# Kernel tuning notes

Measured on AMD Instinct MI355X. Metric: run time of the kernel, lower is better.

The kernel has to match this reference:

```python
import jax, jax.numpy as jnp
import numpy as np

NUM_LAYERS = 2
D = 128
H = 4
L = 16  # context window length
EPS = 1e-6


def _ln(x, g, b):
    mu = jnp.mean(x, -1, keepdims=True)
    v = jnp.mean((x - mu) ** 2, -1, keepdims=True)
    return (x - mu) / jnp.sqrt(v + EPS) * g + b


def _lin(x, W, b):
    # torch Linear / 1x1 Conv2d convention: W is [out, in]
    return jnp.einsum('...i,oi->...o', x, W) + b


def _context_attention(x, Lw):
    # x: [b, m, t, d]; front zero-pad time by Lw-1, sliding-window attention.
    # Note: padded zero keys get logit 0 and DO participate in the softmax
    # (faithful to the original, which does not mask the padding).
    b, m, t, d = x.shape
    xp = jnp.pad(x, ((0, 0), (0, 0), (Lw - 1, 0), (0, 0)))
    idx = jnp.arange(t)[:, None] + jnp.arange(Lw)[None, :]  # [t, Lw]
    win = xp[:, :, idx, :]                                   # [b,m,t,Lw,d]
    s = jnp.einsum('bmtd,bmtld->bmtl', x, win) / jnp.sqrt(jnp.asarray(d, x.dtype))
    w = jax.nn.softmax(s, -1)
    return jnp.einsum('bmtl,bmtld->bmtd', w, win)


def _mha(y, Wq, bq, Wk, bk, Wv, bv, Wfc, bfc):
    b, m, t, d = y.shape
    dk = d // H
    q = _lin(y, Wq, bq)   # 1x1 conv == pointwise linear
    k = _lin(y, Wk, bk)
    v = _lin(y, Wv, bv)
    cq = _context_attention(q, L).reshape(b, m, t, H, dk).transpose(0, 1, 3, 2, 4)
    ck = _context_attention(k, L).reshape(b, m, t, H, dk).transpose(0, 1, 3, 2, 4)
    vh = v.reshape(b, m, t, H, dk).transpose(0, 1, 3, 2, 4)  # [b,m,h,t,dk]
    scale = jnp.sqrt(jnp.asarray(dk, y.dtype))
    s = jnp.einsum('bmhqd,bmhkd->bmhqk', cq, ck) / scale
    a = jax.nn.softmax(s, -1)
    x = jnp.einsum('bmhqk,bmhkd->bmhqd', a, vh)   # [b,m,h,t,dk]
    x = x.transpose(0, 1, 3, 2, 4)                # [b,m,t,h,dk]
    # relation attention across assets m
    xr = x.transpose(0, 2, 3, 1, 4)               # [b,t,h,m,dk]
    sr = jnp.einsum('bthqd,bthkd->bthqk', xr, xr) / scale
    ar = jax.nn.softmax(sr, -1)
    xr = jnp.einsum('bthqk,bthkd->bthqd', ar, xr) # [b,t,h,m,dk]
    x = xr.transpose(0, 3, 1, 2, 4)               # [b,m,t,h,dk]
    return _lin(x.reshape(b, m, t, d), Wfc, bfc)


def setup_inputs() -> dict:
    key = jax.random.key(0)
    ks = jax.random.split(key, 16)
    sc = D ** -0.5
    NL = NUM_LAYERS
    inp = {
        'x':   jax.random.normal(ks[0], (2, 32, 512, D), jnp.float32),
        'Wq':  jax.random.normal(ks[1], (NL, D, D)) * sc,
        'bq':  jnp.zeros((NL, D)),
        'Wk':  jax.random.normal(ks[2], (NL, D, D)) * sc,
        'bk':  jnp.zeros((NL, D)),
        'Wv':  jax.random.normal(ks[3], (NL, D, D)) * sc,
        'bv':  jnp.zeros((NL, D)),
        'Wfc': jax.random.normal(ks[4], (NL, D, D)) * sc,
        'bfc': jnp.zeros((NL, D)),
        'W1':  jax.random.normal(ks[5], (NL, 4 * D, D)) * sc,
        'b1':  jnp.zeros((NL, 4 * D)),
        'W2':  jax.random.normal(ks[6], (NL, D, 4 * D)) * (4 * D) ** -0.5,
        'b2':  jnp.zeros((NL, D)),
        'g1':  jnp.ones((NL, D)),  'be1': jnp.zeros((NL, D)),
        'g2':  jnp.ones((NL, D)),  'be2': jnp.zeros((NL, D)),
        'gf':  jnp.ones((D,)),     'bef': jnp.zeros((D,)),
    }
    return inp


def reference(x, Wq, bq, Wk, bk, Wv, bv, Wfc, bfc, W1, b1, W2, b2,
              g1, be1, g2, be2, gf, bef):
    for i in range(NUM_LAYERS):
        # sublayer 0: pre-LN self-attention + residual (dropout=0)
        y = _mha(_ln(x, g1[i], be1[i]), Wq[i], bq[i], Wk[i], bk[i],
                 Wv[i], bv[i], Wfc[i], bfc[i])
        x = x + y
        # sublayer 1: pre-LN FFN + residual
        z = _ln(x, g2[i], be2[i])
        x = x + _lin(jax.nn.relu(_lin(z, W1[i], b1[i])), W2[i], b2[i])
    return _ln(x, gf, bef)
```

## Files before the change

### kernel.cpp

```cpp
#include <hip/hip_runtime.h>
#include <hip/hip_bf16.h>
#include <math.h>

#define B 2
#define M 32
#define T 512
#define D 128
#define H 4
#define DK 32
#define NTOK (B*M*T)

using s16x8 = __attribute__((ext_vector_type(8))) short;
using s16x4 = __attribute__((ext_vector_type(4))) short;
using f32x4 = __attribute__((ext_vector_type(4))) float;

__device__ __forceinline__ short f2bf(float x) {
    union { float f; unsigned u; } a; a.f = x;
    unsigned r = a.u + 0x7fffu + ((a.u >> 16) & 1u);
    return (short)(r >> 16);
}
__device__ __forceinline__ unsigned pkbf(float lo, float hi) {
    union { __hip_bfloat162 h; unsigned u; } c;
    c.h = __float22bfloat162_rn(float2{lo, hi});
    return c.u;
}

__global__ __launch_bounds__(256) void cvt_all_kernel(const float* __restrict__ Wq, const float* __restrict__ Wk,
                                                      const float* __restrict__ Wv, const float* __restrict__ Wfc,
                                                      const float* __restrict__ W1, const float* __restrict__ W2,
                                                      short* __restrict__ dst)
{
    int i = (blockIdx.x * 256 + threadIdx.x) * 4;
    if (i >= 393216) return;
    const float* src; int off;
    if (i < 131072) {
        int wsel = i >> 15; off = i & 32767;
        src = (wsel == 0) ? Wq : (wsel == 1) ? Wk : (wsel == 2) ? Wv : Wfc;
    } else if (i < 262144) { src = W1; off = i - 131072; }
    else                   { src = W2; off = i - 262144; }
    float4 v = *(const float4*)(src + off);
    ushort4 u;
    u.x = (unsigned short)f2bf(v.x); u.y = (unsigned short)f2bf(v.y);
    u.z = (unsigned short)f2bf(v.z); u.w = (unsigned short)f2bf(v.w);
    *(ushort4*)(dst + i) = u;
}

__global__ __launch_bounds__(256) void ln_kernel(const float* __restrict__ in, float* __restrict__ outf,
                                                 const float* __restrict__ g, const float* __restrict__ b)
{
    int wave = threadIdx.x >> 6;
    int lane = threadIdx.x & 63;
    int row  = blockIdx.x * 4 + wave;
    const float* rp = in + (size_t)row * D;
    float v0 = rp[lane], v1 = rp[lane + 64];
    float s = v0 + v1, ss = v0 * v0 + v1 * v1;
    #pragma unroll
    for (int off = 32; off; off >>= 1) { s += __shfl_xor(s, off); ss += __shfl_xor(ss, off); }
    float mu  = s * (1.0f / 128.0f);
    float var = ss * (1.0f / 128.0f) - mu * mu;
    float rs  = rsqrtf(var + 1e-6f);
    float* op = outf + (size_t)row * D;
    op[lane]      = (v0 - mu) * rs * g[lane]      + b[lane];
    op[lane + 64] = (v1 - mu) * rs * g[lane + 64] + b[lane + 64];
}

#define KP 136

#define LN_STAGE(XPTR, GPTR, BEPTR)                                              \
    {                                                                            \
        const float* xp = (XPTR) + (size_t)(rowBase + sr) * D + sq * 32;         \
        float4 xv[8];                                                            \
        _Pragma("unroll")                                                        \
        for (int j = 0; j < 8; j++) xv[j] = *(const float4*)(xp + j * 4);        \
        float s = 0.0f, ss = 0.0f;                                               \
        _Pragma("unroll")                                                        \
        for (int j = 0; j < 8; j++) {                                            \
            s  += xv[j].x + xv[j].y + xv[j].z + xv[j].w;                         \
            ss += xv[j].x*xv[j].x + xv[j].y*xv[j].y + xv[j].z*xv[j].z + xv[j].w*xv[j].w; \
        }                                                                        \
        s  += __shfl_xor(s, 1);  s  += __shfl_xor(s, 2);                         \
        ss += __shfl_xor(ss, 1); ss += __shfl_xor(ss, 2);                        \
        float mu  = s * (1.0f / 128.0f);                                         \
        float var = ss * (1.0f / 128.0f) - mu * mu;                              \
        float rs  = rsqrtf(var + 1e-6f);                                         \
        const float* gp  = (GPTR) + sq * 32;                                     \
        const float* bep = (BEPTR) + sq * 32;                                    \
        short* asd = &As[sr * KP + sq * 32];                                     \
        _Pragma("unroll")                                                        \
        for (int c = 0; c < 4; c++) {                                            \
            float4 a0 = xv[2*c], a1 = xv[2*c+1];                                 \
            float4 g0 = *(const float4*)(gp + c * 8);                            \
            float4 g1 = *(const float4*)(gp + c * 8 + 4);                        \
            float4 b0 = *(const float4*)(bep + c * 8);                           \
            float4 b1 = *(const float4*)(bep + c * 8 + 4);                       \
            union { unsigned u[4]; s16x8 v8; } pu;                               \
            pu.u[0] = pkbf((a0.x-mu)*rs*g0.x+b0.x, (a0.y-mu)*rs*g0.y+b0.y);      \
            pu.u[1] = pkbf((a0.z-mu)*rs*g0.z+b0.z, (a0.w-mu)*rs*g0.w+b0.w);      \
            pu.u[2] = pkbf((a1.x-mu)*rs*g1.x+b1.x, (a1.y-mu)*rs*g1.y+b1.y);      \
            pu.u[3] = pkbf((a1.z-mu)*rs*g1.z+b1.z, (a1.w-mu)*rs*g1.w+b1.w);      \
            *(s16x8*)(asd + c * 8) = pu.v8;                                      \
        }                                                                        \
    }

__global__ __launch_bounds__(512) void qkv_ln_kernel(const float* __restrict__ X,
                                                     const float* __restrict__ g, const float* __restrict__ be,
                                                     const short* __restrict__ Wq, const short* __restrict__ Wk,
                                                     const short* __restrict__ Wv,
                                                     const float* __restrict__ bq, const float* __restrict__ bk,
                                                     const float* __restrict__ bv,
                                                     short* __restrict__ Qo, short* __restrict__ Ko,
                                                     short* __restrict__ Vo)
{
    __shared__ short As[128 * KP];
    __shared__ short Ws[3][128 * KP];
    const int tid = threadIdx.x;
    const int rowBase = blockIdx.x * 128;
    const int sr = tid >> 2, sq = tid & 3;
    const int w = tid >> 6, l = tid & 63;
    const int lg = l >> 4, lr = l & 15;
    const int wr = w >> 2, wc = w & 3;

    const short* wsrc[3] = { Wq, Wk, Wv };
    const float* bsrc[3] = { bq, bk, bv };
    short*       osrc[3] = { Qo, Ko, Vo };

    #pragma unroll
    for (int gsel = 0; gsel < 3; gsel++) {
        const short* wp = wsrc[gsel] + (size_t)sr * D + sq * 32;
        short* wsd = &Ws[gsel][sr * KP + sq * 32];
        #pragma unroll
        for (int i = 0; i < 4; i++) *(s16x8*)(wsd + i * 8) = *(const s16x8*)(wp + i * 8);
    }
    LN_STAGE(X, g, be)
    __syncthreads();

    for (int gsel = 0; gsel < 3; gsel++) {
        f32x4 acc[4][2];
        #pragma unroll
        for (int qi = 0; qi < 4; qi++)
            #pragma unroll
            for (int nj = 0; nj < 2; nj++)
                acc[qi][nj] = (f32x4){0.0f, 0.0f, 0.0f, 0.0f};
        #pragma unroll
        for (int kk = 0; kk < 4; kk++) {
            s16x8 af[4], bfr[2];
            #pragma unroll
            for (int qi = 0; qi < 4; qi++)
                af[qi] = *(const s16x8*)&As[(wr * 64 + qi * 16 + lr) * KP + kk * 32 + lg * 8];
            #pragma unroll
            for (int nj = 0; nj < 2; nj++)
                bfr[nj] = *(const s16x8*)&Ws[gsel][(wc * 32 + nj * 16 + lr) * KP + kk * 32 + lg * 8];
            #pragma unroll
            for (int qi = 0; qi < 4; qi++)
                #pragma unroll
                for (int nj = 0; nj < 2; nj++)
                    acc[qi][nj] = __builtin_amdgcn_mfma_f32_16x16x32_bf16(af[qi], bfr[nj], acc[qi][nj], 0, 0, 0);
        }
        #pragma unroll
        for (int nj = 0; nj < 2; nj++) {
            int col = wc * 32 + nj * 16 + lr;
            float bb = bsrc[gsel][col];
            #pragma unroll
            for (int qi = 0; qi < 4; qi++) {
                #pragma unroll
                for (int rr = 0; rr < 4; rr++) {
                    int row = rowBase + wr * 64 + qi * 16 + lg * 4 + rr;
                    osrc[gsel][(size_t)row * D + col] = f2bf(acc[qi][nj][rr] + bb);
                }
            }
        }
    }
}

__global__ __launch_bounds__(512) void mlp1_ln_kernel(const float* __restrict__ X,
                                                      const float* __restrict__ g, const float* __restrict__ be,
                                                      const short* __restrict__ W1, const float* __restrict__ b1,
                                                      short* __restrict__ Hb)
{
    __shared__ short As[128 * KP];
    __shared__ short Ws[128 * KP];
    const int tid = threadIdx.x;
    const int rowBase = blockIdx.x * 128;
    const int sr = tid >> 2, sq = tid & 3;
    const int w = tid >> 6, l = tid & 63;
    const int lg = l >> 4, lr = l & 15;
    const int wr = w >> 2, wc = w & 3;

    LN_STAGE(X, g, be)

    for (int ct = 0; ct < 4; ct++) {
        s16x8 wv4[4];
        const short* wp = W1 + (size_t)(ct * 128 + sr) * D + sq * 32;
        #pragma unroll
        for (int i = 0; i < 4; i++) wv4[i] = *(const s16x8*)(wp + i * 8);
        __syncthreads();
        short* wsd = &Ws[sr * KP + sq * 32];
        #pragma unroll
        for (int i = 0; i < 4; i++) *(s16x8*)(wsd + i * 8) = wv4[i];
        __syncthreads();

        f32x4 acc[4][2];
        #pragma unroll
        for (int qi = 0; qi < 4; qi++)
            #pragma unroll
            for (int nj = 0; nj < 2; nj++)
                acc[qi][nj] = (f32x4){0.0f, 0.0f, 0.0f, 0.0f};
        #pragma unroll
        for (int kk = 0; kk < 4; kk++) {
            s16x8 af[4], bfr[2];
            #pragma unroll
            for (int qi = 0; qi < 4; qi++)
                af[qi] = *(const s16x8*)&As[(wr * 64 + qi * 16 + lr) * KP + kk * 32 + lg * 8];
            #pragma unroll
            for (int nj = 0; nj < 2; nj++)
                bfr[nj] = *(const s16x8*)&Ws[(wc * 32 + nj * 16 + lr) * KP + kk * 32 + lg * 8];
            #pragma unroll
            for (int qi = 0; qi < 4; qi++)
                #pragma unroll
                for (int nj = 0; nj < 2; nj++)
                    acc[qi][nj] = __builtin_amdgcn_mfma_f32_16x16x32_bf16(af[qi], bfr[nj], acc[qi][nj], 0, 0, 0);
        }
        #pragma unroll
        for (int nj = 0; nj < 2; nj++) {
            int col = ct * 128 + wc * 32 + nj * 16 + lr;
            float bb = b1[col];
            #pragma unroll
            for (int qi = 0; qi < 4; qi++) {
                #pragma unroll
                for (int rr = 0; rr < 4; rr++) {
                    int row = rowBase + wr * 64 + qi * 16 + lg * 4 + rr;
                    Hb[(size_t)row * 512 + col] = f2bf(fmaxf(acc[qi][nj][rr] + bb, 0.0f));
                }
            }
        }
    }
}

template<int DIN>
__global__ __launch_bounds__(512) void gemm_bf16_kernel(const short* __restrict__ A, const short* __restrict__ W,
                                                        const float* __restrict__ bias, const float* __restrict__ res,
                                                        float* __restrict__ outf, int Dout)
{
    __shared__ short As[128 * KP];
    __shared__ short Ws[128 * KP];
    const int tid = threadIdx.x;
    const int rowBase = blockIdx.y * 128;
    const int colBase = blockIdx.x * 128;
    const int sr = tid >> 2, sq = tid & 3;
    const int w = tid >> 6, l = tid & 63;
    const int lg = l >> 4, lr = l & 15;
    const int wr = w >> 2, wc = w & 3;

    f32x4 acc[4][2];
    #pragma unroll
    for (int qi = 0; qi < 4; qi++)
        #pragma unroll
        for (int nj = 0; nj < 2; nj++)
            acc[qi][nj] = (f32x4){0.0f, 0.0f, 0.0f, 0.0f};

    const short* ap = A + (size_t)(rowBase + sr) * DIN + sq * 32;
    const short* wp = W + (size_t)(colBase + sr) * DIN + sq * 32;
    short* asd = &As[sr * KP + sq * 32];
    short* wsd = &Ws[sr * KP + sq * 32];

    #pragma unroll
    for (int kt = 0; kt < DIN / 128; kt++) {
        s16x8 av[4], wv[4];
        #pragma unroll
        for (int i = 0; i < 4; i++) {
            av[i] = *(const s16x8*)(ap + kt * 128 + i * 8);
            wv[i] = *(const s16x8*)(wp + kt * 128 + i * 8);
        }
        if (kt) __syncthreads();
        #pragma unroll
        for (int i = 0; i < 4; i++) {
            *(s16x8*)(asd + i * 8) = av[i];
            *(s16x8*)(wsd + i * 8) = wv[i];
        }
        __syncthreads();
        #pragma unroll
        for (int kk = 0; kk < 4; kk++) {
            s16x8 af[4], bfr[2];
            #pragma unroll
            for (int qi = 0; qi < 4; qi++)
                af[qi] = *(const s16x8*)&As[(wr * 64 + qi * 16 + lr) * KP + kk * 32 + lg * 8];
            #pragma unroll
            for (int nj = 0; nj < 2; nj++)
                bfr[nj] = *(const s16x8*)&Ws[(wc * 32 + nj * 16 + lr) * KP + kk * 32 + lg * 8];
            #pragma unroll
            for (int qi = 0; qi < 4; qi++)
                #pragma unroll
                for (int nj = 0; nj < 2; nj++)
                    acc[qi][nj] = __builtin_amdgcn_mfma_f32_16x16x32_bf16(af[qi], bfr[nj], acc[qi][nj], 0, 0, 0);
        }
    }

    #pragma unroll
    for (int nj = 0; nj < 2; nj++) {
        int col = colBase + wc * 32 + nj * 16 + lr;
        float bb = bias[col];
        #pragma unroll
        for (int qi = 0; qi < 4; qi++) {
            #pragma unroll
            for (int rr = 0; rr < 4; rr++) {
                int row = rowBase + wr * 64 + qi * 16 + lg * 4 + rr;
                size_t o = (size_t)row * Dout + col;
                outf[o] = acc[qi][nj][rr] + bb + res[o];
            }
        }
    }
}

#define XSP 136
#define XTP 84
__global__ __launch_bounds__(256) void ctx_mfma_kernel(const short* __restrict__ in0, short* __restrict__ out0,
                                                       const short* __restrict__ in1, short* __restrict__ out1)
{
    __shared__ short Xs[80 * XSP];
    __shared__ short Xt[128 * XTP];

    const short* in  = blockIdx.y ? in1 : in0;
    short*       out = blockIdx.y ? out1 : out0;
    int bm = blockIdx.x >> 3;
    int t0 = (blockIdx.x & 7) * 64;
    int tid = threadIdx.x;
    const short* base = in + (size_t)bm * T * D;

    #pragma unroll
    for (int it = 0; it < 5; it++) {
        int idx = it * 256 + tid;
        int row = idx >> 4, c16 = idx & 15;
        int t = t0 - 16 + row;
        s16x8 v = {0, 0, 0, 0, 0, 0, 0, 0};
        if (t >= 0) v = *(const s16x8*)(base + (size_t)t * D + c16 * 8);
        *(s16x8*)&Xs[row * XSP + c16 * 8] = v;
    }
    __syncthreads();
    #pragma unroll
    for (int it = 0; it < 5; it++) {
        int task = it * 256 + tid;
        int g = task / 80, row = task % 80;
        s16x8 v = *(const s16x8*)&Xs[row * XSP + g * 8];
        #pragma unroll
        for (int j = 0; j < 8; j++) Xt[(g * 8 + j) * XTP + row] = v[j];
    }
    __syncthreads();

    int w = tid >> 6, l = tid & 63;
    int lg = l >> 4, lr = l & 15;
    f32x4 zacc = {0.0f, 0.0f, 0.0f, 0.0f};
    const float C1 = 0.0883883476483184f * 1.4426950408889634f;

    s16x8 qf[4];
    #pragma unroll
    for (int kd = 0; kd < 4; kd++)
        qf[kd] = *(const s16x8*)&Xs[(16 + w * 16 + lr) * XSP + kd * 32 + lg * 8];

    f32x4 sacc[2];
    #pragma unroll
    for (int s = 0; s < 2; s++) {
        f32x4 a = zacc;
        #pragma unroll
        for (int kd = 0; kd < 4; kd++) {
            s16x8 kf = *(const s16x8*)&Xs[(w * 16 + s * 16 + lr) * XSP + kd * 32 + lg * 8];
            a = __builtin_amdgcn_mfma_f32_16x16x32_bf16(kf, qf[kd], a, 0, 0, 0);
        }
        sacc[s] = a;
    }

    float p[2][4];
    float mx = -1e30f;
    #pragma unroll
    for (int s = 0; s < 2; s++)
        #pragma unroll
        for (int r = 0; r < 4; r++) {
            int dlt = s * 16 + lg * 4 + r - 16 - lr;
            float val = (dlt >= -15 && dlt <= 0) ? sacc[s][r] : -1e30f;
            p[s][r] = val;
            mx = fmaxf(mx, val);
        }
    mx = fmaxf(mx, __shfl_xor(mx, 16));
    mx = fmaxf(mx, __shfl_xor(mx, 32));
    float mc = mx * C1;
    float ps = 0.0f;
    #pragma unroll
    for (int s = 0; s < 2; s++)
        #pragma unroll
        for (int r = 0; r < 4; r++) {
            float e = exp2f(fmaf(p[s][r], C1, -mc));
            p[s][r] = e;
            ps += e;
        }
    ps += __shfl_xor(ps, 16);
    ps += __shfl_xor(ps, 32);

    union { unsigned u[4]; s16x8 v8; } pu;
    pu.u[0] = pkbf(p[0][0], p[0][1]);
    pu.u[1] = pkbf(p[0][2], p[0][3]);
    pu.u[2] = pkbf(p[1][0], p[1][1]);
    pu.u[3] = pkbf(p[1][2], p[1][3]);
    s16x8 pf = pu.v8;

    float rl = 1.0f / ps;
    short* op = out + (size_t)(bm * T + t0 + w * 16 + lr) * D;
    #pragma unroll
    for (int dt = 0; dt < 8; dt++) {
        const short* vb = &Xt[(dt * 16 + lr) * XTP + w * 16 + lg * 4];
        s16x4 a = *(const s16x4*)(vb);
        s16x4 b = *(const s16x4*)(vb + 16);
        s16x8 vf = __builtin_shufflevector(a, b, 0, 1, 2, 3, 4, 5, 6, 7);
        f32x4 Oa = __builtin_amdgcn_mfma_f32_16x16x32_bf16(vf, pf, zacc, 0, 0, 0);
        union { unsigned u[2]; ushort4 s4; } ou;
        ou.u[0] = pkbf(Oa[0] * rl, Oa[1] * rl);
        ou.u[1] = pkbf(Oa[2] * rl, Oa[3] * rl);
        *(ushort4*)(op + dt * 16 + lg * 4) = ou.s4;
    }
}

#define KPAD 40
#define VTP  520
__global__ __launch_bounds__(1024) void attn_mfma_kernel(const short* __restrict__ q, const short* __restrict__ k,
                                                         const short* __restrict__ v, short* __restrict__ out)
{
    __shared__ short Ks[512 * KPAD];
    __shared__ short Vt[32 * VTP];

    int h  = blockIdx.x & 3;
    int bm = blockIdx.x >> 2;
    int tid = threadIdx.x;
    size_t headoff = (size_t)(bm * T) * D + h * DK;

    {
        int row = tid >> 1, half = tid & 1;
        const s16x8* kp8 = (const s16x8*)(k + headoff + (size_t)row * D + half * 16);
        s16x8 k0 = kp8[0], k1 = kp8[1];
        short* kd = &Ks[row * KPAD + half * 16];
        *(s16x8*)(kd)     = k0;
        *(s16x8*)(kd + 8) = k1;
        const s16x8* vp8 = (const s16x8*)(v + headoff + (size_t)row * D + half * 16);
        s16x8 v0 = vp8[0], v1 = vp8[1];
        #pragma unroll
        for (int d = 0; d < 8; d++) {
            Vt[(half * 16 + d) * VTP + row]     = v0[d];
            Vt[(half * 16 + 8 + d) * VTP + row] = v1[d];
        }
    }
    __syncthreads();

    int w = tid >> 6, l = tid & 63;
    int lg = l >> 4, lr = l & 15;
    int qw = w * 32;

    s16x8 qf[2];
    #pragma unroll
    for (int qi = 0; qi < 2; qi++)
        qf[qi] = *(const s16x8*)(q + headoff + (size_t)(qw + qi * 16 + lr) * D + lg * 8);

    f32x4 Oa[2][2];
    float lrow[2];
    #pragma unroll
    for (int qi = 0; qi < 2; qi++) {
        lrow[qi] = 0.0f;
        #pragma unroll
        for (int r = 0; r < 4; r++) { Oa[qi][0][r] = 0.0f; Oa[qi][1][r] = 0.0f; }
    }
    const float C1 = 0.17677669529663689f * 1.4426950408889634f;
    f32x4 zacc = {0.0f, 0.0f, 0.0f, 0.0f};

    for (int kt = 0; kt < 8; kt++) {
        int kb = kt * 64;
        s16x8 kf[2][2];
        #pragma unroll
        for (int s = 0; s < 2; s++)
            #pragma unroll
            for (int hh = 0; hh < 2; hh++)
                kf[s][hh] = *(const s16x8*)&Ks[(kb + s * 32 + hh * 16 + lr) * KPAD + lg * 8];
        s16x8 vf[2][2];
        #pragma unroll
        for (int dh = 0; dh < 2; dh++)
            #pragma unroll
            for (int s = 0; s < 2; s++) {
                const short* vb = &Vt[(dh * 16 + lr) * VTP + kb + s * 32 + lg * 4];
                s16x4 a = *(const s16x4*)(vb);
                s16x4 b = *(const s16x4*)(vb + 16);
                vf[dh][s] = __builtin_shufflevector(a, b, 0, 1, 2, 3, 4, 5, 6, 7);
            }
        #pragma unroll
        for (int qi = 0; qi < 2; qi++) {
            f32x4 sa[2][2];
            #pragma unroll
            for (int s = 0; s < 2; s++)
                #pragma unroll
                for (int hh = 0; hh < 2; hh++)
                    sa[s][hh] = __builtin_amdgcn_mfma_f32_16x16x32_bf16(kf[s][hh], qf[qi], zacc, 0, 0, 0);
            float p[2][8];
            float ps = 0.0f;
            #pragma unroll
            for (int s = 0; s < 2; s++)
                #pragma unroll
                for (int hh = 0; hh < 2; hh++)
                    #pragma unroll
                    for (int r = 0; r < 4; r++) {
                        float e = exp2f(sa[s][hh][r] * C1);
                        p[s][hh * 4 + r] = e;
                        ps += e;
                    }
            lrow[qi] += ps;
            s16x8 pf[2];
            #pragma unroll
            for (int s = 0; s < 2; s++) {
                union { unsigned u[4]; s16x8 v8; } pu;
                pu.u[0] = pkbf(p[s][0], p[s][1]);
                pu.u[1] = pkbf(p[s][2], p[s][3]);
                pu.u[2] = pkbf(p[s][4], p[s][5]);
                pu.u[3] = pkbf(p[s][6], p[s][7]);
                pf[s] = pu.v8;
            }
            #pragma unroll
            for (int dh = 0; dh < 2; dh++)
                #pragma unroll
                for (int s = 0; s < 2; s++)
                    Oa[qi][dh] = __builtin_amdgcn_mfma_f32_16x16x32_bf16(vf[dh][s], pf[s], Oa[qi][dh], 0, 0, 0);
        }
    }

    #pragma unroll
    for (int qi = 0; qi < 2; qi++) {
        float lv = lrow[qi];
        lv += __shfl_xor(lv, 16);
        lv += __shfl_xor(lv, 32);
        float rl = 1.0f / lv;
        int qrow = qw + qi * 16 + lr;
        short* op = out + headoff + (size_t)qrow * D;
        #pragma unroll
        for (int dh = 0; dh < 2; dh++) {
            union { unsigned u[2]; ushort4 s4; } ou;
            ou.u[0] = pkbf(Oa[qi][dh][0] * rl, Oa[qi][dh][1] * rl);
            ou.u[1] = pkbf(Oa[qi][dh][2] * rl, Oa[qi][dh][3] * rl);
            *(ushort4*)(op + dh * 16 + lg * 4) = ou.s4;
        }
    }
}

#define CXP 136
#define CTP 36
__global__ __launch_bounds__(256) void crossm_mfma_kernel(const short* __restrict__ in, short* __restrict__ out)
{
    __shared__ short Xs[32 * CXP];
    __shared__ short Xt[128 * CTP];
    int b = blockIdx.x >> 9;
    int t = blockIdx.x & 511;
    int tid = threadIdx.x;

    #pragma unroll
    for (int it = 0; it < 2; it++) {
        int idx = it * 256 + tid;
        int m = idx >> 4, c16 = idx & 15;
        s16x8 v = *(const s16x8*)(in + (size_t)((b * M + m) * T + t) * D + c16 * 8);
        *(s16x8*)&Xs[m * CXP + c16 * 8] = v;
    }
    __syncthreads();
    #pragma unroll
    for (int it = 0; it < 2; it++) {
        int task = it * 256 + tid;
        int g = task >> 5, m = task & 31;
        s16x8 v = *(const s16x8*)&Xs[m * CXP + g * 8];
        #pragma unroll
        for (int j = 0; j < 8; j++) Xt[(g * 8 + j) * CTP + m] = v[j];
    }
    __syncthreads();

    int h = tid >> 6, l = tid & 63;
    int lg = l >> 4, lr = l & 15;
    f32x4 zacc = {0.0f, 0.0f, 0.0f, 0.0f};
    const float C1 = 0.17677669529663689f * 1.4426950408889634f;

    s16x8 xf[2];
    #pragma unroll
    for (int i = 0; i < 2; i++)
        xf[i] = *(const s16x8*)&Xs[(i * 16 + lr) * CXP + h * 32 + lg * 8];

    f32x4 sacc[2][2];
    #pragma unroll
    for (int kt = 0; kt < 2; kt++)
        #pragma unroll
        for (int qt = 0; qt < 2; qt++)
            sacc[kt][qt] = __builtin_amdgcn_mfma_f32_16x16x32_bf16(xf[kt], xf[qt], zacc, 0, 0, 0);

    s16x8 pf[2];
    float rl[2];
    #pragma unroll
    for (int qt = 0; qt < 2; qt++) {
        float p[2][4];
        float ps = 0.0f;
        #pragma unroll
        for (int kt = 0; kt < 2; kt++)
            #pragma unroll
            for (int r = 0; r < 4; r++) {
                float e = exp2f(sacc[kt][qt][r] * C1);
                p[kt][r] = e;
                ps += e;
            }
        ps += __shfl_xor(ps, 16);
        ps += __shfl_xor(ps, 32);
        rl[qt] = 1.0f / ps;
        union { unsigned u[4]; s16x8 v8; } pu;
        pu.u[0] = pkbf(p[0][0], p[0][1]);
        pu.u[1] = pkbf(p[0][2], p[0][3]);
        pu.u[2] = pkbf(p[1][0], p[1][1]);
        pu.u[3] = pkbf(p[1][2], p[1][3]);
        pf[qt] = pu.v8;
    }

    #pragma unroll
    for (int qt = 0; qt < 2; qt++) {
        int qm = qt * 16 + lr;
        short* op = out + (size_t)((b * M + qm) * T + t) * D + h * 32;
        #pragma unroll
        for (int dt = 0; dt < 2; dt++) {
            const short* vb = &Xt[(h * 32 + dt * 16 + lr) * CTP + lg * 4];
            s16x4 a = *(const s16x4*)(vb);
            s16x4 bb = *(const s16x4*)(vb + 16);
            s16x8 vf = __builtin_shufflevector(a, bb, 0, 1, 2, 3, 4, 5, 6, 7);
            f32x4 Oa = __builtin_amdgcn_mfma_f32_16x16x32_bf16(vf, pf[qt], zacc, 0, 0, 0);
            union { unsigned u[2]; ushort4 s4; } ou;
            ou.u[0] = pkbf(Oa[0] * rl[qt], Oa[1] * rl[qt]);
            ou.u[1] = pkbf(Oa[2] * rl[qt], Oa[3] * rl[qt]);
            *(ushort4*)(op + dt * 16 + lg * 4) = ou.s4;
        }
    }
}

extern "C" void kernel_launch(void* const* d_in, const int* in_sizes, int n_in,
                              void* d_out, int out_size, void* d_ws, size_t ws_size,
                              hipStream_t stream)
{
    (void)in_sizes; (void)n_in; (void)out_size; (void)ws_size;
    const float* xin = (const float*)d_in[0];
    const float* Wq  = (const float*)d_in[1];
    const float* bq  = (const float*)d_in[2];
    const float* Wk  = (const float*)d_in[3];
    const float* bk  = (const float*)d_in[4];
    const float* Wv  = (const float*)d_in[5];
    const float* bv  = (const float*)d_in[6];
    const float* Wfc = (const float*)d_in[7];
    const float* bfc = (const float*)d_in[8];
    const float* W1  = (const float*)d_in[9];
    const float* b1  = (const float*)d_in[10];
    const float* W2  = (const float*)d_in[11];
    const float* b2  = (const float*)d_in[12];
    const float* g1  = (const float*)d_in[13];
    const float* be1 = (const float*)d_in[14];
    const float* g2  = (const float*)d_in[15];
    const float* be2 = (const float*)d_in[16];
    const float* gf  = (const float*)d_in[17];
    const float* bef = (const float*)d_in[18];

    float* X = (float*)d_out;
    char* wsb = (char*)d_ws;
    const size_t SEGB = (size_t)NTOK * D * sizeof(float);
    const size_t SEGH = SEGB / 2;
    short* Qpb = (short*)(wsb + SEGH);
    short* Kpb = (short*)(wsb + 2 * SEGH);
    short* Vbf = (short*)(wsb + 3 * SEGH);
    short* CQb = (short*)(wsb + 4 * SEGH);
    short* CKb = (short*)(wsb + 5 * SEGH);
    short* Hbf = (short*)(wsb);

    short* Wall = (short*)(wsb + 6 * SEGH);
    short* Wqb  = Wall;
    short* Wkb  = Wall + 32768;
    short* Wvb  = Wall + 65536;
    short* Wfcb = Wall + 98304;
    short* W1b  = Wall + 131072;
    short* W2b  = Wall + 262144;

    cvt_all_kernel<<<384, 256, 0, stream>>>(Wq, Wk, Wv, Wfc, W1, W2, Wall);

    for (int i = 0; i < 2; i++) {
        const float* xi  = i ? X : xin;
        qkv_ln_kernel<<<NTOK / 128, 512, 0, stream>>>(xi, g1 + i * D, be1 + i * D,
                                                      Wqb + i * D * D, Wkb + i * D * D, Wvb + i * D * D,
                                                      bq + i * D, bk + i * D, bv + i * D,
                                                      Qpb, Kpb, Vbf);
        ctx_mfma_kernel<<<dim3(B * M * (T / 64), 2), 256, 0, stream>>>(Qpb, CQb, Kpb, CKb);
        attn_mfma_kernel<<<B * M * H, 1024, 0, stream>>>(CQb, CKb, Vbf, Qpb);
        crossm_mfma_kernel<<<B * T, 256, 0, stream>>>(Qpb, Kpb);
        gemm_bf16_kernel<128><<<dim3(1, NTOK / 128), 512, 0, stream>>>(Kpb, Wfcb + i * D * D, bfc + i * D, xi, X, D);
        mlp1_ln_kernel<<<NTOK / 128, 512, 0, stream>>>(X, g2 + i * D, be2 + i * D,
                                                       W1b + i * 4 * D * D, b1 + i * 4 * D, Hbf);
        gemm_bf16_kernel<512><<<dim3(1, NTOK / 128), 512, 0, stream>>>(Hbf, W2b + i * 4 * D * D, b2 + i * D, X, X, D);
    }
    ln_kernel<<<NTOK / 4, 256, 0, stream>>>(X, X, gf, bef);
}
```

Measured before the change: 228.0 us.

## Fuse FFN up and down projections into one kernel with hidden tile in LDS

Merges the LN+W1+ReLU kernel and the W2 GEMM+residual kernel into a single kernel. Each block handles 64 rows and keeps the 64x512 bf16 hidden activation in shared memory instead of writing it to global and reading it back. The first W1 tile load overlaps with the LayerNorm stage, and W2 tiles stream through the same shared buffer. This removes a launch and the hidden-tensor global round trip, at the cost of a larger LDS footprint per block, smaller row tiles, and extra barriers per tile.

```diff
diff --git a/kernel.cpp b/kernel.cpp
--- a/kernel.cpp
+++ b/kernel.cpp
@@ -172,66 +172,102 @@
     }
 }
 
-__global__ __launch_bounds__(512) void mlp1_ln_kernel(const float* __restrict__ X,
-                                                      const float* __restrict__ g, const float* __restrict__ be,
-                                                      const short* __restrict__ W1, const float* __restrict__ b1,
-                                                      short* __restrict__ Hb)
-{
-    __shared__ short As[128 * KP];
+#define HP 520
+__global__ __launch_bounds__(512) void mlp_ln_kernel(const float* __restrict__ X,
+                                                     const float* __restrict__ g, const float* __restrict__ be,
+                                                     const short* __restrict__ W1, const float* __restrict__ b1,
+                                                     const short* __restrict__ W2, const float* __restrict__ b2,
+                                                     float* __restrict__ Xout)
+{
+    __shared__ short As[64 * KP];
+    __shared__ short Hs[64 * HP];
     __shared__ short Ws[128 * KP];
     const int tid = threadIdx.x;
-    const int rowBase = blockIdx.x * 128;
-    const int sr = tid >> 2, sq = tid & 3;
+    const int rowBase = blockIdx.x * 64;
     const int w = tid >> 6, l = tid & 63;
     const int lg = l >> 4, lr = l & 15;
-    const int wr = w >> 2, wc = w & 3;
-
-    LN_STAGE(X, g, be)
+
+    if (tid < 256) {
+        const int sr = tid >> 2, sq = tid & 3;
+        LN_STAGE(X, g, be)
+    } else {
+        int t2 = tid - 256;
+        int r = t2 >> 1, hh = t2 & 1;
+        const short* p = W1 + (size_t)r * D + hh * 64;
+        short* d2 = &Ws[r * KP + hh * 64];
+        #pragma unroll
+        for (int i = 0; i < 8; i++) *(s16x8*)(d2 + i * 8) = *(const s16x8*)(p + i * 8);
+    }
+    __syncthreads();
+
+    const int swr = tid >> 2, swq = tid & 3;
 
     for (int ct = 0; ct < 4; ct++) {
-        s16x8 wv4[4];
-        const short* wp = W1 + (size_t)(ct * 128 + sr) * D + sq * 32;
-        #pragma unroll
-        for (int i = 0; i < 4; i++) wv4[i] = *(const s16x8*)(wp + i * 8);
+        f32x4 hacc[4];
+        #pragma unroll
+        for (int qi = 0; qi < 4; qi++) hacc[qi] = (f32x4){0.0f, 0.0f, 0.0f, 0.0f};
+        #pragma unroll
+        for (int kk = 0; kk < 4; kk++) {
+            s16x8 bf = *(const s16x8*)&Ws[(w * 16 + lr) * KP + kk * 32 + lg * 8];
+            #pragma unroll
+            for (int qi = 0; qi < 4; qi++) {
+                s16x8 af = *(const s16x8*)&As[(qi * 16 + lr) * KP + kk * 32 + lg * 8];
+                hacc[qi] = __builtin_amdgcn_mfma_f32_16x16x32_bf16(af, bf, hacc[qi], 0, 0, 0);
+            }
+        }
         __syncthreads();
-        short* wsd = &Ws[sr * KP + sq * 32];
-        #pragma unroll
-        for (int i = 0; i < 4; i++) *(s16x8*)(wsd + i * 8) = wv4[i];
+        {
+            const short* p = (ct < 3) ? (W1 + (size_t)((ct + 1) * 128 + swr) * D + swq * 32)
+                                      : (W2 + (size_t)swr * 512 + swq * 32);
+            short* d2 = &Ws[swr * KP + swq * 32];
+            #pragma unroll
+            for (int i = 0; i < 4; i++) *(s16x8*)(d2 + i * 8) = *(const s16x8*)(p + i * 8);
+        }
+        int col = ct * 128 + w * 16 + lr;
+        float bb = b1[col];
+        #pragma unroll
+        for (int qi = 0; qi < 4; qi++) {
+            #pragma unroll
+            for (int rr = 0; rr < 4; rr++) {
+                int hrow = qi * 16 + lg * 4 + rr;
+                Hs[hrow * HP + col] = f2bf(fmaxf(hacc[qi][rr] + bb, 0.0f));
+            }
+        }
         __syncthreads();
-
-        f32x4 acc[4][2];
-        #pragma unroll
-        for (int qi = 0; qi < 4; qi++)
-            #pragma unroll
-            for (int nj = 0; nj < 2; nj++)
-                acc[qi][nj] = (f32x4){0.0f, 0.0f, 0.0f, 0.0f};
+    }
+
+    f32x4 acc[4];
+    #pragma unroll
+    for (int qi = 0; qi < 4; qi++) acc[qi] = (f32x4){0.0f, 0.0f, 0.0f, 0.0f};
+    for (int kt = 0; kt < 4; kt++) {
         #pragma unroll
         for (int kk = 0; kk < 4; kk++) {
-            s16x8 af[4], bfr[2];
-            #pragma unroll
-            for (int qi = 0; qi < 4; qi++)
-                af[qi] = *(const s16x8*)&As[(wr * 64 + qi * 16 + lr) * KP + kk * 32 + lg * 8];
-            #pragma unroll
-            for (int nj = 0; nj < 2; nj++)
-                bfr[nj] = *(const s16x8*)&Ws[(wc * 32 + nj * 16 + lr) * KP + kk * 32 + lg * 8];
-            #pragma unroll
-            for (int qi = 0; qi < 4; qi++)
-                #pragma unroll
-                for (int nj = 0; nj < 2; nj++)
-                    acc[qi][nj] = __builtin_amdgcn_mfma_f32_16x16x32_bf16(af[qi], bfr[nj], acc[qi][nj], 0, 0, 0);
-        }
-        #pragma unroll
-        for (int nj = 0; nj < 2; nj++) {
-            int col = ct * 128 + wc * 32 + nj * 16 + lr;
-            float bb = b1[col];
+            s16x8 bf = *(const s16x8*)&Ws[(w * 16 + lr) * KP + kk * 32 + lg * 8];
             #pragma unroll
             for (int qi = 0; qi < 4; qi++) {
-                #pragma unroll
-                for (int rr = 0; rr < 4; rr++) {
-                    int row = rowBase + wr * 64 + qi * 16 + lg * 4 + rr;
-                    Hb[(size_t)row * 512 + col] = f2bf(fmaxf(acc[qi][nj][rr] + bb, 0.0f));
-                }
+                s16x8 af = *(const s16x8*)&Hs[(qi * 16 + lr) * HP + kt * 128 + kk * 32 + lg * 8];
+                acc[qi] = __builtin_amdgcn_mfma_f32_16x16x32_bf16(af, bf, acc[qi], 0, 0, 0);
             }
+        }
+        if (kt < 3) {
+            __syncthreads();
+            const short* p = W2 + (size_t)swr * 512 + (kt + 1) * 128 + swq * 32;
+            short* d2 = &Ws[swr * KP + swq * 32];
+            #pragma unroll
+            for (int i = 0; i < 4; i++) *(s16x8*)(d2 + i * 8) = *(const s16x8*)(p + i * 8);
+            __syncthreads();
+        }
+    }
+
+    int col = w * 16 + lr;
+    float bb2 = b2[col];
+    #pragma unroll
+    for (int qi = 0; qi < 4; qi++) {
+        #pragma unroll
+        for (int rr = 0; rr < 4; rr++) {
+            int row = rowBase + qi * 16 + lg * 4 + rr;
+            size_t o = (size_t)row * D + col;
+            Xout[o] = acc[qi][rr] + bb2 + Xout[o];
         }
     }
 }
@@ -665,7 +701,6 @@
     short* Vbf = (short*)(wsb + 3 * SEGH);
     short* CQb = (short*)(wsb + 4 * SEGH);
     short* CKb = (short*)(wsb + 5 * SEGH);
-    short* Hbf = (short*)(wsb);
 
     short* Wall = (short*)(wsb + 6 * SEGH);
     short* Wqb  = Wall;
@@ -687,9 +722,9 @@
         attn_mfma_kernel<<<B * M * H, 1024, 0, stream>>>(CQb, CKb, Vbf, Qpb);
         crossm_mfma_kernel<<<B * T, 256, 0, stream>>>(Qpb, Kpb);
         gemm_bf16_kernel<128><<<dim3(1, NTOK / 128), 512, 0, stream>>>(Kpb, Wfcb + i * D * D, bfc + i * D, xi, X, D);
-        mlp1_ln_kernel<<<NTOK / 128, 512, 0, stream>>>(X, g2 + i * D, be2 + i * D,
-                                                       W1b + i * 4 * D * D, b1 + i * 4 * D, Hbf);
-        gemm_bf16_kernel<512><<<dim3(1, NTOK / 128), 512, 0, stream>>>(Hbf, W2b + i * 4 * D * D, b2 + i * D, X, X, D);
+        mlp_ln_kernel<<<NTOK / 64, 512, 0, stream>>>(X, g2 + i * D, be2 + i * D,
+                                                     W1b + i * 4 * D * D, b1 + i * 4 * D,
+                                                     W2b + i * 4 * D * D, b2 + i * D, X);
     }
     ln_kernel<<<NTOK / 4, 256, 0, stream>>>(X, X, gf, bef);
 }
```

New measurement: 230.6 us. About the same (+1.1%).

## Fuse FFN up and down projections into one kernel, keeping hidden activations in registers

Applied to the files above, without the earlier changes.

Merges the LN+W1+ReLU kernel and the W2 GEMM into one kernel. Each wave computes the hidden tile with MFMA in transposed form, packs the ReLU outputs to bf16 directly as the B operand of the second MFMA, and accumulates the output across hidden chunks. This removes the write and re-read of the 32768x512 bf16 hidden buffer and one kernel launch. In exchange it adds more shared memory per block, synchronisations on each hidden chunk, and stalls from the serialised weight reloads.

```diff
diff --git a/kernel.cpp b/kernel.cpp
--- a/kernel.cpp
+++ b/kernel.cpp
@@ -172,67 +172,112 @@
     }
 }
 
-__global__ __launch_bounds__(512) void mlp1_ln_kernel(const float* __restrict__ X,
-                                                      const float* __restrict__ g, const float* __restrict__ be,
-                                                      const short* __restrict__ W1, const float* __restrict__ b1,
-                                                      short* __restrict__ Hb)
+__global__ __launch_bounds__(512) void mlp_ln_kernel(const float* __restrict__ X,
+                                                     const float* __restrict__ g, const float* __restrict__ be,
+                                                     const short* __restrict__ W1, const float* __restrict__ b1,
+                                                     const short* __restrict__ W2, const float* __restrict__ b2,
+                                                     float* __restrict__ Xout)
 {
     __shared__ short As[128 * KP];
-    __shared__ short Ws[128 * KP];
+    __shared__ short W1s[128 * KP];
+    __shared__ short W2s[128 * KP];
     const int tid = threadIdx.x;
     const int rowBase = blockIdx.x * 128;
     const int sr = tid >> 2, sq = tid & 3;
     const int w = tid >> 6, l = tid & 63;
     const int lg = l >> 4, lr = l & 15;
-    const int wr = w >> 2, wc = w & 3;
+    f32x4 zacc = {0.0f, 0.0f, 0.0f, 0.0f};
 
     LN_STAGE(X, g, be)
-
-    for (int ct = 0; ct < 4; ct++) {
-        s16x8 wv4[4];
-        const short* wp = W1 + (size_t)(ct * 128 + sr) * D + sq * 32;
-        #pragma unroll
-        for (int i = 0; i < 4; i++) wv4[i] = *(const s16x8*)(wp + i * 8);
-        __syncthreads();
-        short* wsd = &Ws[sr * KP + sq * 32];
-        #pragma unroll
-        for (int i = 0; i < 4; i++) *(s16x8*)(wsd + i * 8) = wv4[i];
-        __syncthreads();
-
-        f32x4 acc[4][2];
-        #pragma unroll
-        for (int qi = 0; qi < 4; qi++)
-            #pragma unroll
-            for (int nj = 0; nj < 2; nj++)
-                acc[qi][nj] = (f32x4){0.0f, 0.0f, 0.0f, 0.0f};
-        #pragma unroll
-        for (int kk = 0; kk < 4; kk++) {
-            s16x8 af[4], bfr[2];
-            #pragma unroll
-            for (int qi = 0; qi < 4; qi++)
-                af[qi] = *(const s16x8*)&As[(wr * 64 + qi * 16 + lr) * KP + kk * 32 + lg * 8];
-            #pragma unroll
-            for (int nj = 0; nj < 2; nj++)
-                bfr[nj] = *(const s16x8*)&Ws[(wc * 32 + nj * 16 + lr) * KP + kk * 32 + lg * 8];
-            #pragma unroll
-            for (int qi = 0; qi < 4; qi++)
+    {
+        const short* p1 = W1 + (size_t)sr * D + sq * 32;
+        short* d1 = &W1s[sr * KP + sq * 32];
+        #pragma unroll
+        for (int i = 0; i < 4; i++) *(s16x8*)(d1 + i * 8) = *(const s16x8*)(p1 + i * 8);
+        const short* p2 = W2 + (size_t)sr * 512 + sq * 32;
+        short* d2 = &W2s[sr * KP + sq * 32];
+        #pragma unroll
+        for (int i = 0; i < 4; i++) *(s16x8*)(d2 + i * 8) = *(const s16x8*)(p2 + i * 8);
+    }
+    __syncthreads();
+
+    s16x8 xf[4];
+    #pragma unroll
+    for (int kd = 0; kd < 4; kd++)
+        xf[kd] = *(const s16x8*)&As[(w * 16 + lr) * KP + kd * 32 + lg * 8];
+
+    f32x4 oacc[8];
+    #pragma unroll
+    for (int ot = 0; ot < 8; ot++) oacc[ot] = zacc;
+
+    for (int gg = 0; gg < 4; gg++) {
+        #pragma unroll
+        for (int c = 0; c < 4; c++) {
+            f32x4 hacc[2];
+            #pragma unroll
+            for (int hh = 0; hh < 2; hh++) {
+                f32x4 a = zacc;
                 #pragma unroll
-                for (int nj = 0; nj < 2; nj++)
-                    acc[qi][nj] = __builtin_amdgcn_mfma_f32_16x16x32_bf16(af[qi], bfr[nj], acc[qi][nj], 0, 0, 0);
-        }
-        #pragma unroll
-        for (int nj = 0; nj < 2; nj++) {
-            int col = ct * 128 + wc * 32 + nj * 16 + lr;
-            float bb = b1[col];
-            #pragma unroll
-            for (int qi = 0; qi < 4; qi++) {
-                #pragma unroll
-                for (int rr = 0; rr < 4; rr++) {
-                    int row = rowBase + wr * 64 + qi * 16 + lg * 4 + rr;
-                    Hb[(size_t)row * 512 + col] = f2bf(fmaxf(acc[qi][nj][rr] + bb, 0.0f));
+                for (int kd = 0; kd < 4; kd++) {
+                    s16x8 wf = *(const s16x8*)&W1s[(c * 32 + hh * 16 + lr) * KP + kd * 32 + lg * 8];
+                    a = __builtin_amdgcn_mfma_f32_16x16x32_bf16(wf, xf[kd], a, 0, 0, 0);
                 }
+                hacc[hh] = a;
             }
-        }
+            int hbase = gg * 128 + c * 32;
+            float4 b1v0 = *(const float4*)&b1[hbase + lg * 4];
+            float4 b1v1 = *(const float4*)&b1[hbase + 16 + lg * 4];
+            float p[8];
+            p[0] = fmaxf(hacc[0][0] + b1v0.x, 0.0f);
+            p[1] = fmaxf(hacc[0][1] + b1v0.y, 0.0f);
+            p[2] = fmaxf(hacc[0][2] + b1v0.z, 0.0f);
+            p[3] = fmaxf(hacc[0][3] + b1v0.w, 0.0f);
+            p[4] = fmaxf(hacc[1][0] + b1v1.x, 0.0f);
+            p[5] = fmaxf(hacc[1][1] + b1v1.y, 0.0f);
+            p[6] = fmaxf(hacc[1][2] + b1v1.z, 0.0f);
+            p[7] = fmaxf(hacc[1][3] + b1v1.w, 0.0f);
+            union { unsigned u[4]; s16x8 v8; } pu;
+            pu.u[0] = pkbf(p[0], p[1]);
+            pu.u[1] = pkbf(p[2], p[3]);
+            pu.u[2] = pkbf(p[4], p[5]);
+            pu.u[3] = pkbf(p[6], p[7]);
+            s16x8 pf = pu.v8;
+            #pragma unroll
+            for (int ot = 0; ot < 8; ot++) {
+                const short* vb = &W2s[(ot * 16 + lr) * KP + c * 32 + lg * 4];
+                s16x4 a4 = *(const s16x4*)(vb);
+                s16x4 b4 = *(const s16x4*)(vb + 16);
+                s16x8 vf = __builtin_shufflevector(a4, b4, 0, 1, 2, 3, 4, 5, 6, 7);
+                oacc[ot] = __builtin_amdgcn_mfma_f32_16x16x32_bf16(vf, pf, oacc[ot], 0, 0, 0);
+            }
+        }
+        if (gg < 3) {
+            __syncthreads();
+            const short* p1 = W1 + (size_t)((gg + 1) * 128 + sr) * D + sq * 32;
+            short* d1 = &W1s[sr * KP + sq * 32];
+            #pragma unroll
+            for (int i = 0; i < 4; i++) *(s16x8*)(d1 + i * 8) = *(const s16x8*)(p1 + i * 8);
+            const short* p2 = W2 + (size_t)sr * 512 + (gg + 1) * 128 + sq * 32;
+            short* d2 = &W2s[sr * KP + sq * 32];
+            #pragma unroll
+            for (int i = 0; i < 4; i++) *(s16x8*)(d2 + i * 8) = *(const s16x8*)(p2 + i * 8);
+            __syncthreads();
+        }
+    }
+
+    int xrow = rowBase + w * 16 + lr;
+    float* xp = Xout + (size_t)xrow * D;
+    #pragma unroll
+    for (int ot = 0; ot < 8; ot++) {
+        int col = ot * 16 + lg * 4;
+        float4 res = *(const float4*)(xp + col);
+        float4 bv  = *(const float4*)(b2 + col);
+        float4 o;
+        o.x = oacc[ot][0] + bv.x + res.x;
+        o.y = oacc[ot][1] + bv.y + res.y;
+        o.z = oacc[ot][2] + bv.z + res.z;
+        o.w = oacc[ot][3] + bv.w + res.w;
+        *(float4*)(xp + col) = o;
     }
 }
 
@@ -665,7 +710,6 @@
     short* Vbf = (short*)(wsb + 3 * SEGH);
     short* CQb = (short*)(wsb + 4 * SEGH);
     short* CKb = (short*)(wsb + 5 * SEGH);
-    short* Hbf = (short*)(wsb);
 
     short* Wall = (short*)(wsb + 6 * SEGH);
     short* Wqb  = Wall;
@@ -687,9 +731,9 @@
         attn_mfma_kernel<<<B * M * H, 1024, 0, stream>>>(CQb, CKb, Vbf, Qpb);
         crossm_mfma_kernel<<<B * T, 256, 0, stream>>>(Qpb, Kpb);
         gemm_bf16_kernel<128><<<dim3(1, NTOK / 128), 512, 0, stream>>>(Kpb, Wfcb + i * D * D, bfc + i * D, xi, X, D);
-        mlp1_ln_kernel<<<NTOK / 128, 512, 0, stream>>>(X, g2 + i * D, be2 + i * D,
-                                                       W1b + i * 4 * D * D, b1 + i * 4 * D, Hbf);
-        gemm_bf16_kernel<512><<<dim3(1, NTOK / 128), 512, 0, stream>>>(Hbf, W2b + i * 4 * D * D, b2 + i * D, X, X, D);
+        mlp_ln_kernel<<<NTOK / 128, 512, 0, stream>>>(X, g2 + i * D, be2 + i * D,
+                                                      W1b + i * 4 * D * D, b1 + i * 4 * D,
+                                                      W2b + i * 4 * D * D, b2 + i * D, X);
     }
     ln_kernel<<<NTOK / 4, 256, 0, stream>>>(X, X, gf, bef);
 }
```

New measurement: 217.1 us, median of 3. -4.8%, faster.
